# Kernel optimization log

Hardware: AMD Instinct MI355X
Metric: run time of the kernel (lower is better)

The kernel has to match this reference:

```python
import jax, jax.numpy as jnp
import numpy as np

P = 9    # patch_size (number of shifts per axis)
DP = 1   # dilation_patch (pixel step per shift)


def setup_inputs() -> dict:
    key = jax.random.key(0)
    k1, k2 = jax.random.split(key)
    input1 = jax.random.normal(k1, (4, 256, 96, 128), dtype=jnp.float32)
    input2 = jax.random.normal(k2, (4, 256, 96, 128), dtype=jnp.float32)
    return {"input1": input1, "input2": input2}


def _correlation(input1, input2):
    # Faithful to iter_spatial_correlation_sample with kernel_size=1, stride=1,
    # padding=0, dilation=1: offsets are integer pixel shifts, and bilinear
    # grid_sample (align_corners=True, zeros outside) at integer coordinates is
    # exactly a zero-padded integer shift of input2.
    b, c, h, w = input2.shape
    off = DP * ((P - 1) // 2)  # center offset in pixels
    pad2 = jnp.pad(input2, ((0, 0), (0, 0), (off, off), (off, off)))
    rows = []
    for i in range(P):          # small fixed loop over patch offsets (81 total)
        cols = []
        for j in range(P):
            # window = input2 shifted by (dy, dx) = (i*DP - off, j*DP - off)
            win = jax.lax.dynamic_slice(pad2, (0, 0, i * DP, j * DP), (b, c, h, w))
            cols.append(jnp.einsum('bchw,bchw->bhw', input1, win))
        rows.append(jnp.stack(cols, axis=1))  # [b, P, h, w]
    return jnp.stack(rows, axis=1)            # [b, P, P, h, w]


def reference(input1, input2):
    return _correlation(input1, input2)
```

## Files before the change

### kernel.cpp

```cpp
#include <hip/hip_runtime.h>

#define BB 4
#define CC 256
#define HH 96
#define WW 128
#define PP 9
#define OFF 4
#define CCH 16
#define NPAIR (CCH / 2)
#define NCH (CC / CCH)
#define TPB 288
#define TW 72
#define XCOLS 64

typedef _Float16 h2 __attribute__((ext_vector_type(2)));

__device__ __forceinline__ h2 u2h(unsigned u) { union { unsigned u; h2 h; } x; x.u = u; return x.h; }

#if __has_builtin(__builtin_amdgcn_fdot2)
__device__ __forceinline__ float dot2(h2 a, h2 b, float c) { return __builtin_amdgcn_fdot2(a, b, c, false); }
#else
__device__ __forceinline__ float dot2(h2 a, h2 b, float c) { return c + (float)a[0] * (float)b[0] + (float)a[1] * (float)b[1]; }
#endif

__device__ __forceinline__ unsigned pk(float a, float b) {
#if __has_builtin(__builtin_amdgcn_cvt_pkrtz)
  auto r = __builtin_amdgcn_cvt_pkrtz(a, b);
  unsigned u; __builtin_memcpy(&u, &r, 4); return u;
#else
  h2 h; h[0] = (_Float16)a; h[1] = (_Float16)b;
  unsigned u; __builtin_memcpy(&u, &h, 4); return u;
#endif
}

__global__ __launch_bounds__(TPB, 4) void corr_kernel(const float* __restrict__ in1,
                                                      const float* __restrict__ in2,
                                                      float* __restrict__ out) {
  __shared__ unsigned s2[NPAIR][PP][TW];
  __shared__ unsigned s1[NPAIR][XCOLS];

  const int bx = blockIdx.x;
  const int xcd = bx & 7;
  const int slot = bx >> 3;
  const int xh = slot & 1;
  const int s3 = slot >> 1;
  const int b = s3 / 12;
  const int h = xcd * 12 + (s3 % 12);
  const int xbase = xh * XCOLS;

  const int tid = threadIdx.x;
  const int dy = tid >> 5;
  const int pxg = tid & 31;
  const int L0 = pxg << 1;

  const int sp = tid / 36;
  const int sc2 = tid - sp * 36;
  const int sL = sc2 << 1;
  const int sgx = xbase - OFF + sL;
  const bool colv = (sgx >= 0) && (sgx < WW);
  const int rlo = (h >= OFF) ? 0 : (OFF - h);
  const int rhi = (PP < HH + OFF - h) ? PP : (HH + OFF - h);

  const int plane = HH * WW;
  const long base_b = (long)b * CC * plane;

  const float* p2a = in2 + base_b + (long)(2 * sp) * plane + (long)(h - OFF) * WW + sgx;
  const float* p2b = p2a + plane;
  const int i1p = tid >> 5, i1c = tid & 31;
  const float* p1a = in1 + base_b + (long)(2 * i1p) * plane + h * WW + xbase + (i1c << 1);
  const float* p1b = p1a + plane;

  for (int i = tid; i < NPAIR * PP * TW; i += TPB) ((unsigned*)s2)[i] = 0u;

  float acc[2][PP];
#pragma unroll
  for (int px = 0; px < 2; ++px)
#pragma unroll
    for (int dx = 0; dx < PP; ++dx) acc[px][dx] = 0.f;

  float2 fa[PP], fb[PP], ga, gb;

  if (colv) {
#pragma unroll
    for (int r = 0; r < PP; ++r)
      if (r >= rlo && r < rhi) {
        fa[r] = *(const float2*)(p2a + r * WW);
        fb[r] = *(const float2*)(p2b + r * WW);
      }
  }
  if (tid < NPAIR * 32) { ga = *(const float2*)p1a; gb = *(const float2*)p1b; }
  __syncthreads();

#pragma unroll 1
  for (int c = 0; c < NCH; ++c) {
    if (colv) {
#pragma unroll
      for (int r = 0; r < PP; ++r)
        if (r >= rlo && r < rhi)
          *(uint2*)&s2[sp][r][sL] = make_uint2(pk(fa[r].x, fb[r].x), pk(fa[r].y, fb[r].y));
    }
    if (tid < NPAIR * 32)
      *(uint2*)&s1[i1p][i1c << 1] = make_uint2(pk(ga.x, gb.x), pk(ga.y, gb.y));
    __syncthreads();

    if (c + 1 < NCH) {
      const long adv = (long)(c + 1) * CCH * plane;
      if (colv) {
#pragma unroll
        for (int r = 0; r < PP; ++r)
          if (r >= rlo && r < rhi) {
            fa[r] = *(const float2*)(p2a + adv + r * WW);
            fb[r] = *(const float2*)(p2b + adv + r * WW);
          }
      }
      if (tid < NPAIR * 32) { ga = *(const float2*)(p1a + adv); gb = *(const float2*)(p1b + adv); }
    }

#pragma unroll
    for (int p = 0; p < NPAIR; ++p) {
      unsigned q[2], w[10];
      *(uint2*)q = *(const uint2*)&s1[p][L0];
#pragma unroll
      for (int i = 0; i < 5; ++i)
        *(uint2*)&w[2 * i] = *(const uint2*)&s2[p][dy][L0 + 2 * i];
#pragma unroll
      for (int px = 0; px < 2; ++px)
#pragma unroll
        for (int dx = 0; dx < PP; ++dx)
          acc[px][dx] = dot2(u2h(w[px + dx]), u2h(q[px]), acc[px][dx]);
    }
    __syncthreads();
  }

  const int gx0 = xbase + L0;
  float* ob = out + ((long)(b * PP + dy) * PP) * plane + h * WW + gx0;
#pragma unroll
  for (int dx = 0; dx < PP; ++dx)
    *(float2*)(ob + (long)dx * plane) = make_float2(acc[0][dx], acc[1][dx]);
}

extern "C" void kernel_launch(void* const* d_in, const int* in_sizes, int n_in,
                              void* d_out, int out_size, void* d_ws, size_t ws_size,
                              hipStream_t stream) {
  const float* in1 = (const float*)d_in[0];
  const float* in2 = (const float*)d_in[1];
  float* out = (float*)d_out;
  corr_kernel<<<dim3(BB * HH * 2), dim3(TPB), 0, stream>>>(in1, in2, out);
}
```

Measured before the change: 160.7 us.

## Split channel reduction across two thread groups per block with LDS reduction

Doubles the block to 576 threads and splits the 256 channels into two halves, each handled by its own 288-thread group with separate LDS tiles. Each group loops over half as many channel chunks, and at the end the second group writes its partial sums to shared memory, where the first group adds them before writing the output. The aim is to shorten each block's serial channel loop and add more waves to hide latency. The cost is double the LDS per block, fewer resident blocks, and an extra reduction step with a barrier.

New measurement: 204.7 us. 1.27x slower.

```diff
diff --git a/kernel.cpp b/kernel.cpp
--- a/kernel.cpp
+++ b/kernel.cpp
@@ -6,10 +6,12 @@
 #define WW 128
 #define PP 9
 #define OFF 4
+#define CG 2
+#define CPB (CC / CG)
 #define CCH 16
 #define NPAIR (CCH / 2)
-#define NCH (CC / CCH)
-#define TPB 288
+#define NCH (CPB / CCH)
+#define TPB 576
 #define TW 72
 #define XCOLS 64
 
@@ -33,11 +35,11 @@
 #endif
 }
 
-__global__ __launch_bounds__(TPB, 4) void corr_kernel(const float* __restrict__ in1,
+__global__ __launch_bounds__(TPB, 7) void corr_kernel(const float* __restrict__ in1,
                                                       const float* __restrict__ in2,
                                                       float* __restrict__ out) {
-  __shared__ unsigned s2[NPAIR][PP][TW];
-  __shared__ unsigned s1[NPAIR][XCOLS];
+  __shared__ unsigned s2[CG][NPAIR][PP][TW];
+  __shared__ unsigned s1[CG][NPAIR][XCOLS];
 
   const int bx = blockIdx.x;
   const int xcd = bx & 7;
@@ -49,12 +51,14 @@
   const int xbase = xh * XCOLS;
 
   const int tid = threadIdx.x;
-  const int dy = tid >> 5;
-  const int pxg = tid & 31;
+  const int cg = (tid >= 288) ? 1 : 0;
+  const int ltid = tid - 288 * cg;
+  const int dy = ltid >> 5;
+  const int pxg = ltid & 31;
   const int L0 = pxg << 1;
 
-  const int sp = tid / 36;
-  const int sc2 = tid - sp * 36;
+  const int sp = ltid / 36;
+  const int sc2 = ltid - sp * 36;
   const int sL = sc2 << 1;
   const int sgx = xbase - OFF + sL;
   const bool colv = (sgx >= 0) && (sgx < WW);
@@ -64,13 +68,14 @@
   const int plane = HH * WW;
   const long base_b = (long)b * CC * plane;
 
-  const float* p2a = in2 + base_b + (long)(2 * sp) * plane + (long)(h - OFF) * WW + sgx;
+  const float* p2a = in2 + base_b + (long)(cg * CPB + 2 * sp) * plane + (long)(h - OFF) * WW + sgx;
   const float* p2b = p2a + plane;
-  const int i1p = tid >> 5, i1c = tid & 31;
-  const float* p1a = in1 + base_b + (long)(2 * i1p) * plane + h * WW + xbase + (i1c << 1);
+  const int i1p = ltid >> 5, i1c = ltid & 31;
+  const float* p1a = in1 + base_b + (long)(cg * CPB + 2 * i1p) * plane + h * WW + xbase + (i1c << 1);
   const float* p1b = p1a + plane;
+  const bool in1v = (ltid < NPAIR * 32);
 
-  for (int i = tid; i < NPAIR * PP * TW; i += TPB) ((unsigned*)s2)[i] = 0u;
+  for (int i = tid; i < CG * NPAIR * PP * TW; i += TPB) ((unsigned*)s2)[i] = 0u;
 
   float acc[2][PP];
 #pragma unroll
@@ -88,7 +93,7 @@
         fb[r] = *(const float2*)(p2b + r * WW);
       }
   }
-  if (tid < NPAIR * 32) { ga = *(const float2*)p1a; gb = *(const float2*)p1b; }
+  if (in1v) { ga = *(const float2*)p1a; gb = *(const float2*)p1b; }
   __syncthreads();
 
 #pragma unroll 1
@@ -97,10 +102,10 @@
 #pragma unroll
       for (int r = 0; r < PP; ++r)
         if (r >= rlo && r < rhi)
-          *(uint2*)&s2[sp][r][sL] = make_uint2(pk(fa[r].x, fb[r].x), pk(fa[r].y, fb[r].y));
+          *(uint2*)&s2[cg][sp][r][sL] = make_uint2(pk(fa[r].x, fb[r].x), pk(fa[r].y, fb[r].y));
     }
-    if (tid < NPAIR * 32)
-      *(uint2*)&s1[i1p][i1c << 1] = make_uint2(pk(ga.x, gb.x), pk(ga.y, gb.y));
+    if (in1v)
+      *(uint2*)&s1[cg][i1p][i1c << 1] = make_uint2(pk(ga.x, gb.x), pk(ga.y, gb.y));
     __syncthreads();
 
     if (c + 1 < NCH) {
@@ -113,16 +118,16 @@
             fb[r] = *(const float2*)(p2b + adv + r * WW);
           }
       }
-      if (tid < NPAIR * 32) { ga = *(const float2*)(p1a + adv); gb = *(const float2*)(p1b + adv); }
+      if (in1v) { ga = *(const float2*)(p1a + adv); gb = *(const float2*)(p1b + adv); }
     }
 
 #pragma unroll
     for (int p = 0; p < NPAIR; ++p) {
       unsigned q[2], w[10];
-      *(uint2*)q = *(const uint2*)&s1[p][L0];
+      *(uint2*)q = *(const uint2*)&s1[cg][p][L0];
 #pragma unroll
       for (int i = 0; i < 5; ++i)
-        *(uint2*)&w[2 * i] = *(const uint2*)&s2[p][dy][L0 + 2 * i];
+        *(uint2*)&w[2 * i] = *(const uint2*)&s2[cg][p][dy][L0 + 2 * i];
 #pragma unroll
       for (int px = 0; px < 2; ++px)
 #pragma unroll
@@ -132,11 +137,22 @@
     __syncthreads();
   }
 
-  const int gx0 = xbase + L0;
-  float* ob = out + ((long)(b * PP + dy) * PP) * plane + h * WW + gx0;
+  float2* red = (float2*)s2;
+  if (cg) {
 #pragma unroll
-  for (int dx = 0; dx < PP; ++dx)
-    *(float2*)(ob + (long)dx * plane) = make_float2(acc[0][dx], acc[1][dx]);
+    for (int dx = 0; dx < PP; ++dx)
+      red[ltid * PP + dx] = make_float2(acc[0][dx], acc[1][dx]);
+  }
+  __syncthreads();
+  if (!cg) {
+    const int gx0 = xbase + L0;
+    float* ob = out + ((long)(b * PP + dy) * PP) * plane + h * WW + gx0;
+#pragma unroll
+    for (int dx = 0; dx < PP; ++dx) {
+      const float2 v = red[ltid * PP + dx];
+      *(float2*)(ob + (long)dx * plane) = make_float2(acc[0][dx] + v.x, acc[1][dx] + v.y);
+    }
+  }
 }
 
 extern "C" void kernel_launch(void* const* d_in, const int* in_sizes, int n_in,
```

## Double-buffer LDS tiles and make global loads branch-free with clamped rows

Applied to the files above, without the earlier changes.

Shared-memory tiles are double-buffered so the next channel chunk is written into the alternate buffer after compute. This removes one barrier per chunk and overlaps staging with the dot-product work. Global loads become unconditional by clamping row and column addresses, and only the shared-memory stores stay predicated, which removes divergent branches around the loads. In exchange, LDS use doubles, occupancy drops (launch bounds lowered from 4 to 3 waves per SIMD), and redundant out-of-range loads are issued.

After: 260.6 us. 62.1% more time.

```diff
diff --git a/kernel.cpp b/kernel.cpp
--- a/kernel.cpp
+++ b/kernel.cpp
@@ -33,11 +33,11 @@
 #endif
 }
 
-__global__ __launch_bounds__(TPB, 4) void corr_kernel(const float* __restrict__ in1,
+__global__ __launch_bounds__(TPB, 3) void corr_kernel(const float* __restrict__ in1,
                                                       const float* __restrict__ in2,
                                                       float* __restrict__ out) {
-  __shared__ unsigned s2[NPAIR][PP][TW];
-  __shared__ unsigned s1[NPAIR][XCOLS];
+  __shared__ unsigned s2[2][NPAIR][PP][TW];
+  __shared__ unsigned s1[2][NPAIR][XCOLS];
 
   const int bx = blockIdx.x;
   const int xcd = bx & 7;
@@ -58,19 +58,29 @@
   const int sL = sc2 << 1;
   const int sgx = xbase - OFF + sL;
   const bool colv = (sgx >= 0) && (sgx < WW);
+  const int sgxc = colv ? sgx : xbase;
   const int rlo = (h >= OFF) ? 0 : (OFF - h);
   const int rhi = (PP < HH + OFF - h) ? PP : (HH + OFF - h);
 
   const int plane = HH * WW;
   const long base_b = (long)b * CC * plane;
 
-  const float* p2a = in2 + base_b + (long)(2 * sp) * plane + (long)(h - OFF) * WW + sgx;
+  int rowoff[PP];
+#pragma unroll
+  for (int r = 0; r < PP; ++r) {
+    int hr = h + r - OFF;
+    hr = hr < 0 ? 0 : (hr >= HH ? HH - 1 : hr);
+    rowoff[r] = hr * WW;
+  }
+
+  const float* p2a = in2 + base_b + (long)(2 * sp) * plane + sgxc;
   const float* p2b = p2a + plane;
-  const int i1p = tid >> 5, i1c = tid & 31;
+  const int i1p = (tid >> 5) & 7, i1c = tid & 31;
+  const bool in1v = (tid < NPAIR * 32);
   const float* p1a = in1 + base_b + (long)(2 * i1p) * plane + h * WW + xbase + (i1c << 1);
   const float* p1b = p1a + plane;
 
-  for (int i = tid; i < NPAIR * PP * TW; i += TPB) ((unsigned*)s2)[i] = 0u;
+  for (int i = tid; i < 2 * NPAIR * PP * TW; i += TPB) ((unsigned*)s2)[i] = 0u;
 
   float acc[2][PP];
 #pragma unroll
@@ -80,54 +90,60 @@
 
   float2 fa[PP], fb[PP], ga, gb;
 
+#pragma unroll
+  for (int r = 0; r < PP; ++r) {
+    fa[r] = *(const float2*)(p2a + rowoff[r]);
+    fb[r] = *(const float2*)(p2b + rowoff[r]);
+  }
+  ga = *(const float2*)p1a; gb = *(const float2*)p1b;
+  __syncthreads();
   if (colv) {
 #pragma unroll
     for (int r = 0; r < PP; ++r)
-      if (r >= rlo && r < rhi) {
-        fa[r] = *(const float2*)(p2a + r * WW);
-        fb[r] = *(const float2*)(p2b + r * WW);
-      }
+      if (r >= rlo && r < rhi)
+        *(uint2*)&s2[0][sp][r][sL] = make_uint2(pk(fa[r].x, fb[r].x), pk(fa[r].y, fb[r].y));
   }
-  if (tid < NPAIR * 32) { ga = *(const float2*)p1a; gb = *(const float2*)p1b; }
+  if (in1v)
+    *(uint2*)&s1[0][i1p][i1c << 1] = make_uint2(pk(ga.x, gb.x), pk(ga.y, gb.y));
   __syncthreads();
 
 #pragma unroll 1
   for (int c = 0; c < NCH; ++c) {
-    if (colv) {
-#pragma unroll
-      for (int r = 0; r < PP; ++r)
-        if (r >= rlo && r < rhi)
-          *(uint2*)&s2[sp][r][sL] = make_uint2(pk(fa[r].x, fb[r].x), pk(fa[r].y, fb[r].y));
-    }
-    if (tid < NPAIR * 32)
-      *(uint2*)&s1[i1p][i1c << 1] = make_uint2(pk(ga.x, gb.x), pk(ga.y, gb.y));
-    __syncthreads();
+    const int buf = c & 1;
 
     if (c + 1 < NCH) {
       const long adv = (long)(c + 1) * CCH * plane;
-      if (colv) {
 #pragma unroll
-        for (int r = 0; r < PP; ++r)
-          if (r >= rlo && r < rhi) {
-            fa[r] = *(const float2*)(p2a + adv + r * WW);
-            fb[r] = *(const float2*)(p2b + adv + r * WW);
-          }
+      for (int r = 0; r < PP; ++r) {
+        fa[r] = *(const float2*)(p2a + adv + rowoff[r]);
+        fb[r] = *(const float2*)(p2b + adv + rowoff[r]);
       }
-      if (tid < NPAIR * 32) { ga = *(const float2*)(p1a + adv); gb = *(const float2*)(p1b + adv); }
+      ga = *(const float2*)(p1a + adv); gb = *(const float2*)(p1b + adv);
     }
 
 #pragma unroll
     for (int p = 0; p < NPAIR; ++p) {
       unsigned q[2], w[10];
-      *(uint2*)q = *(const uint2*)&s1[p][L0];
+      *(uint2*)q = *(const uint2*)&s1[buf][p][L0];
 #pragma unroll
       for (int i = 0; i < 5; ++i)
-        *(uint2*)&w[2 * i] = *(const uint2*)&s2[p][dy][L0 + 2 * i];
+        *(uint2*)&w[2 * i] = *(const uint2*)&s2[buf][p][dy][L0 + 2 * i];
 #pragma unroll
       for (int px = 0; px < 2; ++px)
 #pragma unroll
         for (int dx = 0; dx < PP; ++dx)
           acc[px][dx] = dot2(u2h(w[px + dx]), u2h(q[px]), acc[px][dx]);
+    }
+
+    if (c + 1 < NCH) {
+      if (colv) {
+#pragma unroll
+        for (int r = 0; r < PP; ++r)
+          if (r >= rlo && r < rhi)
+            *(uint2*)&s2[buf ^ 1][sp][r][sL] = make_uint2(pk(fa[r].x, fb[r].x), pk(fa[r].y, fb[r].y));
+      }
+      if (in1v)
+        *(uint2*)&s1[buf ^ 1][i1p][i1c << 1] = make_uint2(pk(ga.x, gb.x), pk(ga.y, gb.y));
     }
     __syncthreads();
   }
```

## Process full image row per block with four pixels per thread

Applied to the files above, without the earlier changes.

Each block now covers the full 128-column row instead of half, and each thread computes four adjacent output pixels instead of two. Shared tiles, global loads and stores widen to 128-bit, and the halo overhead per row shrinks, so each loaded input2 value is reused across more dx offsets. The grid halves to 384 blocks and launch bounds drop to 2 waves per SIMD, which lowers parallelism and occupancy in exchange for fewer LDS reads per FMA.

New measurement: 225.8 us. 40.5% more time.

```diff
diff --git a/kernel.cpp b/kernel.cpp
--- a/kernel.cpp
+++ b/kernel.cpp
@@ -10,8 +10,7 @@
 #define NPAIR (CCH / 2)
 #define NCH (CC / CCH)
 #define TPB 288
-#define TW 72
-#define XCOLS 64
+#define TW 144
 
 typedef _Float16 h2 __attribute__((ext_vector_type(2)));
 
@@ -33,98 +32,99 @@
 #endif
 }
 
-__global__ __launch_bounds__(TPB, 4) void corr_kernel(const float* __restrict__ in1,
+__global__ __launch_bounds__(TPB, 2) void corr_kernel(const float* __restrict__ in1,
                                                       const float* __restrict__ in2,
                                                       float* __restrict__ out) {
   __shared__ unsigned s2[NPAIR][PP][TW];
-  __shared__ unsigned s1[NPAIR][XCOLS];
+  __shared__ unsigned s1[NPAIR][WW];
 
   const int bx = blockIdx.x;
   const int xcd = bx & 7;
   const int slot = bx >> 3;
-  const int xh = slot & 1;
-  const int s3 = slot >> 1;
-  const int b = s3 / 12;
-  const int h = xcd * 12 + (s3 % 12);
-  const int xbase = xh * XCOLS;
+  const int b = slot / 12;
+  const int h = xcd * 12 + (slot % 12);
 
   const int tid = threadIdx.x;
   const int dy = tid >> 5;
   const int pxg = tid & 31;
-  const int L0 = pxg << 1;
+  const int L0 = pxg << 2;
 
   const int sp = tid / 36;
-  const int sc2 = tid - sp * 36;
-  const int sL = sc2 << 1;
-  const int sgx = xbase - OFF + sL;
-  const bool colv = (sgx >= 0) && (sgx < WW);
+  const int sq = tid - sp * 36;
+  const bool qv = (sq >= 1) && (sq <= 32);
+  const int x0s = (sq << 2) - OFF;
   const int rlo = (h >= OFF) ? 0 : (OFF - h);
   const int rhi = (PP < HH + OFF - h) ? PP : (HH + OFF - h);
 
   const int plane = HH * WW;
   const long base_b = (long)b * CC * plane;
 
-  const float* p2a = in2 + base_b + (long)(2 * sp) * plane + (long)(h - OFF) * WW + sgx;
+  const float* p2a = in2 + base_b + (long)(2 * sp) * plane + (long)(h - OFF) * WW + x0s;
   const float* p2b = p2a + plane;
-  const int i1p = tid >> 5, i1c = tid & 31;
-  const float* p1a = in1 + base_b + (long)(2 * i1p) * plane + h * WW + xbase + (i1c << 1);
+  const int i1p = (tid >> 5) & 7, i1q = tid & 31;
+  const bool in1v = (tid < NPAIR * 32);
+  const float* p1a = in1 + base_b + (long)(2 * i1p) * plane + h * WW + (i1q << 2);
   const float* p1b = p1a + plane;
 
-  for (int i = tid; i < NPAIR * PP * TW; i += TPB) ((unsigned*)s2)[i] = 0u;
+  for (int i = tid; i < NPAIR * PP * (TW / 4); i += TPB)
+    *(((uint4*)s2) + i) = make_uint4(0u, 0u, 0u, 0u);
 
-  float acc[2][PP];
+  float acc[4][PP];
 #pragma unroll
-  for (int px = 0; px < 2; ++px)
+  for (int px = 0; px < 4; ++px)
 #pragma unroll
     for (int dx = 0; dx < PP; ++dx) acc[px][dx] = 0.f;
 
-  float2 fa[PP], fb[PP], ga, gb;
+  float4 fa[PP], fb[PP], ga, gb;
 
-  if (colv) {
+  if (qv) {
 #pragma unroll
     for (int r = 0; r < PP; ++r)
       if (r >= rlo && r < rhi) {
-        fa[r] = *(const float2*)(p2a + r * WW);
-        fb[r] = *(const float2*)(p2b + r * WW);
+        fa[r] = *(const float4*)(p2a + r * WW);
+        fb[r] = *(const float4*)(p2b + r * WW);
       }
   }
-  if (tid < NPAIR * 32) { ga = *(const float2*)p1a; gb = *(const float2*)p1b; }
+  if (in1v) { ga = *(const float4*)p1a; gb = *(const float4*)p1b; }
   __syncthreads();
 
 #pragma unroll 1
   for (int c = 0; c < NCH; ++c) {
-    if (colv) {
+    if (qv) {
 #pragma unroll
       for (int r = 0; r < PP; ++r)
         if (r >= rlo && r < rhi)
-          *(uint2*)&s2[sp][r][sL] = make_uint2(pk(fa[r].x, fb[r].x), pk(fa[r].y, fb[r].y));
+          *(uint4*)&s2[sp][r][sq << 2] =
+              make_uint4(pk(fa[r].x, fb[r].x), pk(fa[r].y, fb[r].y),
+                         pk(fa[r].z, fb[r].z), pk(fa[r].w, fb[r].w));
     }
-    if (tid < NPAIR * 32)
-      *(uint2*)&s1[i1p][i1c << 1] = make_uint2(pk(ga.x, gb.x), pk(ga.y, gb.y));
+    if (in1v)
+      *(uint4*)&s1[i1p][i1q << 2] =
+          make_uint4(pk(ga.x, gb.x), pk(ga.y, gb.y), pk(ga.z, gb.z), pk(ga.w, gb.w));
     __syncthreads();
 
     if (c + 1 < NCH) {
       const long adv = (long)(c + 1) * CCH * plane;
-      if (colv) {
+      if (qv) {
 #pragma unroll
         for (int r = 0; r < PP; ++r)
           if (r >= rlo && r < rhi) {
-            fa[r] = *(const float2*)(p2a + adv + r * WW);
-            fb[r] = *(const float2*)(p2b + adv + r * WW);
+            fa[r] = *(const float4*)(p2a + adv + r * WW);
+            fb[r] = *(const float4*)(p2b + adv + r * WW);
           }
       }
-      if (tid < NPAIR * 32) { ga = *(const float2*)(p1a + adv); gb = *(const float2*)(p1b + adv); }
+      if (in1v) { ga = *(const float4*)(p1a + adv); gb = *(const float4*)(p1b + adv); }
     }
 
 #pragma unroll
     for (int p = 0; p < NPAIR; ++p) {
-      unsigned q[2], w[10];
-      *(uint2*)q = *(const uint2*)&s1[p][L0];
+      unsigned q[4], w[12];
+      *(uint4*)q = *(const uint4*)&s1[p][L0];
+      *(uint4*)&w[0] = *(const uint4*)&s2[p][dy][L0];
+      *(uint4*)&w[4] = *(const uint4*)&s2[p][dy][L0 + 4];
+      *(uint4*)&w[8] = *(const uint4*)&s2[p][dy][L0 + 8];
 #pragma unroll
-      for (int i = 0; i < 5; ++i)
-        *(uint2*)&w[2 * i] = *(const uint2*)&s2[p][dy][L0 + 2 * i];
-#pragma unroll
-      for (int px = 0; px < 2; ++px)
+      for (int px = 0; px < 4; ++px)
 #pragma unroll
         for (int dx = 0; dx < PP; ++dx)
           acc[px][dx] = dot2(u2h(w[px + dx]), u2h(q[px]), acc[px][dx]);
@@ -132,11 +132,10 @@
     __syncthreads();
   }
 
-  const int gx0 = xbase + L0;
-  float* ob = out + ((long)(b * PP + dy) * PP) * plane + h * WW + gx0;
+  float* ob = out + ((long)(b * PP + dy) * PP) * plane + h * WW + L0;
 #pragma unroll
   for (int dx = 0; dx < PP; ++dx)
-    *(float2*)(ob + (long)dx * plane) = make_float2(acc[0][dx], acc[1][dx]);
+    *(float4*)(ob + (long)dx * plane) = make_float4(acc[0][dx], acc[1][dx], acc[2][dx], acc[3][dx]);
 }
 
 extern "C" void kernel_launch(void* const* d_in, const int* in_sizes, int n_in,
@@ -145,5 +144,5 @@
   const float* in1 = (const float*)d_in[0];
   const float* in2 = (const float*)d_in[1];
   float* out = (float*)d_out;
-  corr_kernel<<<dim3(BB * HH * 2), dim3(TPB), 0, stream>>>(in1, in2, out);
+  corr_kernel<<<dim3(BB * HH), dim3(TPB), 0, stream>>>(in1, in2, out);
 }
```
